# Optimization experiments

Measured on AMD Instinct MI355X. Metric: run time of the kernel, lower is better.

Reference implementation:

```python
import jax, jax.numpy as jnp
import numpy as np

B, T, D, H = 2, 2048, 1024, 16
HD = D // H  # 64
SCALE = 1.0 / np.sqrt(D).astype(np.float32)  # module uses 1/sqrt(mod_dim), not head_dim


def setup_inputs() -> dict:
    key = jax.random.key(0)
    k1, k2, k3 = jax.random.split(key, 3)
    x = jax.random.normal(k1, (B, T, D), dtype=jnp.float32)
    W_attn = jax.random.normal(k2, (3 * D, D), dtype=jnp.float32) * 0.02
    W_out = jax.random.normal(k3, (D, D), dtype=jnp.float32) * 0.02
    return {"x": x, "W_attn": W_attn, "W_out": W_out}


def reference(x, W_attn, W_out):
    b, t, d = x.shape
    # qkv projection (Linear, no bias): x @ W^T
    qkv = jnp.einsum('btd,ed->bte', x, W_attn)  # [b, t, 3d]
    q, k, v = jnp.split(qkv, 3, axis=-1)
    # [b, h, t, hd]
    q = q.reshape(b, t, H, HD).transpose(0, 2, 1, 3)
    k = k.reshape(b, t, H, HD).transpose(0, 2, 1, 3)
    v = v.reshape(b, t, H, HD).transpose(0, 2, 1, 3)
    # raw scores, causal mask applied before scaling (scale*-inf == -inf, so
    # equivalent to the original mask-then-scale order)
    att = jnp.einsum('bhqd,bhkd->bhqk', q, k)
    causal = jnp.tril(jnp.ones((t, t), dtype=bool))
    att = jnp.where(causal[None, None], att * SCALE, -jnp.inf)
    att = jax.nn.softmax(att, axis=-1)
    z = jnp.einsum('bhqk,bhkd->bhqd', att, v)
    z = z.transpose(0, 2, 1, 3).reshape(b, t, d)
    return jnp.einsum('btd,od->bto', z, W_out)
```

## Files before the change

### kernel.cpp

```cpp
#include <hip/hip_runtime.h>
#include <cstddef>

typedef unsigned short u16;
typedef __attribute__((ext_vector_type(4))) float floatx4;
typedef __attribute__((ext_vector_type(8))) short short8;

#define TT 2048
#define DD 1024
#define NH 16
#define ATT_SCALE (1.0f / 32.0f)
#define PSTR 72

__device__ __forceinline__ u16 f2bf(float f) {
  unsigned u = __builtin_bit_cast(unsigned, f);
  u += 0x7fffu + ((u >> 16) & 1u);
  return (u16)(u >> 16);
}

__device__ __forceinline__ void g2l16(const u16* g, u16* l) {
#if __has_builtin(__builtin_amdgcn_global_load_lds)
  __builtin_amdgcn_global_load_lds(
      (const __attribute__((address_space(1))) unsigned int*)g,
      (__attribute__((address_space(3))) unsigned int*)l, 16, 0, 0);
#else
  *(int4*)l = *(const int4*)g;
#endif
}

__device__ __forceinline__ short8 scale_q(short8 q) {
  short8 r;
#pragma unroll
  for (int i = 0; i < 8; ++i) {
    float f = __builtin_bit_cast(float, ((unsigned)(u16)q[i]) << 16) * ATT_SCALE;
    r[i] = (short)f2bf(f);
  }
  return r;
}

__global__ __launch_bounds__(256) void cvt3_kernel(const float* __restrict__ a,
                                                   const float* __restrict__ b,
                                                   const float* __restrict__ c,
                                                   u16* __restrict__ out,
                                                   int na, int nb, int nc) {
  int i = blockIdx.x * 256 + threadIdx.x;
  const float* src;
  int j;
  if (i < na) { src = a; j = i; }
  else if (i < na + nb) { src = b; j = i - na; }
  else if (i < na + nb + nc) { src = c; j = i - na - nb; }
  else return;
  float4 v = ((const float4*)src)[j];
  ((ushort4*)out)[i] = make_ushort4(f2bf(v.x), f2bf(v.y), f2bf(v.z), f2bf(v.w));
}

template <int OUT_BF16, int BN>
__global__ __launch_bounds__(256) void gemm_bt(const u16* __restrict__ A,
                                               const u16* __restrict__ Bm,
                                               void* __restrict__ C,
                                               int M, int N, int K) {
  constexpr int NT = BN / 32;
  __shared__ u16 As[128 * 32];
  __shared__ u16 Bs[BN * 32];
  const int tid = threadIdx.x;
  const int lane = tid & 63;
  const int wave = tid >> 6;
  const int quad = lane >> 4;
  const int l16 = lane & 15;
  const int wm = (wave >> 1) * 64;
  const int wn = (wave & 1) * (BN / 2);
  const int m0 = blockIdx.x * 128;
  const int n0 = blockIdx.y * BN;

  const int srow = wave * 16 + (lane >> 2);
  const int scol = (lane & 3) * 8;
  const int sl = wave * 512 + lane * 8;

  floatx4 acc[4][NT] = {};

  for (int k0 = 0; k0 < K; k0 += 32) {
    __syncthreads();
    g2l16(&A[(size_t)(m0 + srow) * K + k0 + scol], &As[sl]);
    g2l16(&A[(size_t)(m0 + 64 + srow) * K + k0 + scol], &As[2048 + sl]);
    g2l16(&Bm[(size_t)(n0 + srow) * K + k0 + scol], &Bs[sl]);
    if (BN == 128)
      g2l16(&Bm[(size_t)(n0 + 64 + srow) * K + k0 + scol], &Bs[2048 + sl]);
    __syncthreads();

    short8 af[4];
#pragma unroll
    for (int mt = 0; mt < 4; ++mt)
      af[mt] = *(const short8*)&As[(wm + mt * 16 + l16) * 32 + quad * 8];
#pragma unroll
    for (int nt = 0; nt < NT; ++nt) {
      short8 bf = *(const short8*)&Bs[(wn + nt * 16 + l16) * 32 + quad * 8];
#pragma unroll
      for (int mt = 0; mt < 4; ++mt)
        acc[mt][nt] = __builtin_amdgcn_mfma_f32_16x16x32_bf16(af[mt], bf, acc[mt][nt], 0, 0, 0);
    }
  }

#pragma unroll
  for (int mt = 0; mt < 4; ++mt)
#pragma unroll
    for (int nt = 0; nt < NT; ++nt)
#pragma unroll
      for (int r = 0; r < 4; ++r) {
        int gm = m0 + wm + mt * 16 + quad * 4 + r;
        int gn = n0 + wn + nt * 16 + l16;
        float v = acc[mt][nt][r];
        if (OUT_BF16)
          ((u16*)C)[(size_t)gm * N + gn] = f2bf(v);
        else
          ((float*)C)[(size_t)gm * N + gn] = v;
      }
}

__global__ __launch_bounds__(256) void vtrans(const u16* __restrict__ qkv,
                                              u16* __restrict__ vt) {
  __shared__ u16 T[64 * PSTR];
  const int tid = threadIdx.x;
  const int bh = blockIdx.y;
  const int b = bh >> 4, h = bh & 15;
  const int t0 = blockIdx.x * 64;
  const int tr = tid >> 2, c = (tid & 3) * 16;
  const u16* vg = qkv + (size_t)b * TT * 3072 + 2048 + h * 64;
  *(int4*)&T[tr * PSTR + c] = *(const int4*)&vg[(size_t)(t0 + tr) * 3072 + c];
  *(int4*)&T[tr * PSTR + c + 8] = *(const int4*)&vg[(size_t)(t0 + tr) * 3072 + c + 8];
  __syncthreads();
  const int d = tid >> 2, tc = (tid & 3) * 16;
  short8 o0, o1;
#pragma unroll
  for (int j = 0; j < 8; ++j) {
    o0[j] = (short)T[(tc + j) * PSTR + d];
    o1[j] = (short)T[(tc + 8 + j) * PSTR + d];
  }
  u16* dst = vt + ((size_t)bh * 64 + d) * TT + t0 + tc;
  *(short8*)dst = o0;
  *(short8*)(dst + 8) = o1;
}

__global__ __launch_bounds__(256) void attn_flash3(const u16* __restrict__ qkv,
                                                   const u16* __restrict__ vt,
                                                   u16* __restrict__ z) {
  __shared__ u16 Ks[2][64 * PSTR];
  __shared__ u16 Vs[2][64 * PSTR];
  __shared__ u16 Ps[4][2][16 * PSTR];

  const int tid = threadIdx.x;
  const int lane = tid & 63;
  const int wave = tid >> 6;
  const int quad = lane >> 4;
  const int l16 = lane & 15;

  const int p = blockIdx.x;
  const int qtA = p, qtB = 31 - p;
  const int bh = blockIdx.y;
  const int b = bh >> 4, h = bh & 15;

  const size_t bbase = (size_t)b * TT * 3072;
  const u16* qg = qkv + bbase + h * 64;
  const u16* kg = qkv + bbase + 1024 + h * 64;
  const u16* vtg = vt + (size_t)bh * 64 * TT;

  short8 qfA[2], qfB[2];
  {
    const size_t ra = (size_t)(qtA * 64 + wave * 16 + l16) * 3072;
    const size_t rb = (size_t)(qtB * 64 + wave * 16 + l16) * 3072;
    qfA[0] = scale_q(*(const short8*)&qg[ra + quad * 8]);
    qfA[1] = scale_q(*(const short8*)&qg[ra + 32 + quad * 8]);
    qfB[0] = scale_q(*(const short8*)&qg[rb + quad * 8]);
    qfB[1] = scale_q(*(const short8*)&qg[rb + 32 + quad * 8]);
  }

  floatx4 OA[4] = {}, OB[4] = {};
  float psA[4] = {}, psB[4] = {};

  const int str = tid >> 2, sc = (tid & 3) * 16;
  const int nktA = qtA + 1, nktB = qtB + 1;
  const int qrbA = qtA * 64 + wave * 16 + quad * 4;
  const int qrbB = qtB * 64 + wave * 16 + quad * 4;

  {
    int4 k0 = *(const int4*)&kg[(size_t)str * 3072 + sc];
    int4 k1 = *(const int4*)&kg[(size_t)str * 3072 + sc + 8];
    int4 v0 = *(const int4*)&vtg[(size_t)str * TT + sc];
    int4 v1 = *(const int4*)&vtg[(size_t)str * TT + sc + 8];
    *(int4*)&Ks[0][str * PSTR + sc] = k0;
    *(int4*)&Ks[0][str * PSTR + sc + 8] = k1;
    *(int4*)&Vs[0][str * PSTR + sc] = v0;
    *(int4*)&Vs[0][str * PSTR + sc + 8] = v1;
  }
  __syncthreads();

  for (int kt = 0; kt < nktB; ++kt) {
    const int kt0 = kt * 64;
    const int cur = kt & 1, nxt = cur ^ 1;
    const bool pre = (kt + 1 < nktB);

    int4 kr0, kr1, vr0, vr1;
    if (pre) {
      const int kt0n = kt0 + 64;
      kr0 = *(const int4*)&kg[(size_t)(kt0n + str) * 3072 + sc];
      kr1 = *(const int4*)&kg[(size_t)(kt0n + str) * 3072 + sc + 8];
      vr0 = *(const int4*)&vtg[(size_t)str * TT + kt0n + sc];
      vr1 = *(const int4*)&vtg[(size_t)str * TT + kt0n + sc + 8];
    }

    const bool actA = (kt < nktA);

    floatx4 sB[4], sA[4];
#pragma unroll
    for (int nt = 0; nt < 4; ++nt) {
      short8 k0 = *(const short8*)&Ks[cur][(nt * 16 + l16) * PSTR + quad * 8];
      short8 k1 = *(const short8*)&Ks[cur][(nt * 16 + l16) * PSTR + 32 + quad * 8];
      floatx4 zz = {0.f, 0.f, 0.f, 0.f};
      sB[nt] = __builtin_amdgcn_mfma_f32_16x16x32_bf16(qfB[0], k0, zz, 0, 0, 0);
      sB[nt] = __builtin_amdgcn_mfma_f32_16x16x32_bf16(qfB[1], k1, sB[nt], 0, 0, 0);
      if (actA) {
        sA[nt] = __builtin_amdgcn_mfma_f32_16x16x32_bf16(qfA[0], k0, zz, 0, 0, 0);
        sA[nt] = __builtin_amdgcn_mfma_f32_16x16x32_bf16(qfA[1], k1, sA[nt], 0, 0, 0);
      }
    }

    if (kt == qtB) {
#pragma unroll
      for (int nt = 0; nt < 4; ++nt)
#pragma unroll
        for (int r = 0; r < 4; ++r) {
          int kk = kt0 + nt * 16 + l16;
          float pv = (kk <= qrbB + r) ? __expf(sB[nt][r]) : 0.f;
          psB[r] += pv;
          Ps[wave][1][(quad * 4 + r) * PSTR + nt * 16 + l16] = f2bf(pv);
        }
    } else {
#pragma unroll
      for (int nt = 0; nt < 4; ++nt)
#pragma unroll
        for (int r = 0; r < 4; ++r) {
          float pv = __expf(sB[nt][r]);
          psB[r] += pv;
          Ps[wave][1][(quad * 4 + r) * PSTR + nt * 16 + l16] = f2bf(pv);
        }
    }
    if (actA) {
      if (kt == qtA) {
#pragma unroll
        for (int nt = 0; nt < 4; ++nt)
#pragma unroll
          for (int r = 0; r < 4; ++r) {
            int kk = kt0 + nt * 16 + l16;
            float pv = (kk <= qrbA + r) ? __expf(sA[nt][r]) : 0.f;
            psA[r] += pv;
            Ps[wave][0][(quad * 4 + r) * PSTR + nt * 16 + l16] = f2bf(pv);
          }
      } else {
#pragma unroll
        for (int nt = 0; nt < 4; ++nt)
#pragma unroll
          for (int r = 0; r < 4; ++r) {
            float pv = __expf(sA[nt][r]);
            psA[r] += pv;
            Ps[wave][0][(quad * 4 + r) * PSTR + nt * 16 + l16] = f2bf(pv);
          }
      }
    }

    short8 pB0 = *(const short8*)&Ps[wave][1][l16 * PSTR + quad * 8];
    short8 pB1 = *(const short8*)&Ps[wave][1][l16 * PSTR + 32 + quad * 8];
    short8 pA0, pA1;
    if (actA) {
      pA0 = *(const short8*)&Ps[wave][0][l16 * PSTR + quad * 8];
      pA1 = *(const short8*)&Ps[wave][0][l16 * PSTR + 32 + quad * 8];
    }
#pragma unroll
    for (int nt = 0; nt < 4; ++nt) {
      short8 v0 = *(const short8*)&Vs[cur][(nt * 16 + l16) * PSTR + quad * 8];
      short8 v1 = *(const short8*)&Vs[cur][(nt * 16 + l16) * PSTR + 32 + quad * 8];
      OB[nt] = __builtin_amdgcn_mfma_f32_16x16x32_bf16(pB0, v0, OB[nt], 0, 0, 0);
      OB[nt] = __builtin_amdgcn_mfma_f32_16x16x32_bf16(pB1, v1, OB[nt], 0, 0, 0);
      if (actA) {
        OA[nt] = __builtin_amdgcn_mfma_f32_16x16x32_bf16(pA0, v0, OA[nt], 0, 0, 0);
        OA[nt] = __builtin_amdgcn_mfma_f32_16x16x32_bf16(pA1, v1, OA[nt], 0, 0, 0);
      }
    }

    __syncthreads();
    if (pre) {
      *(int4*)&Ks[nxt][str * PSTR + sc] = kr0;
      *(int4*)&Ks[nxt][str * PSTR + sc + 8] = kr1;
      *(int4*)&Vs[nxt][str * PSTR + sc] = vr0;
      *(int4*)&Vs[nxt][str * PSTR + sc + 8] = vr1;
      __syncthreads();
    }
  }

#pragma unroll
  for (int off = 1; off < 16; off <<= 1)
#pragma unroll
    for (int r = 0; r < 4; ++r) {
      psA[r] += __shfl_xor(psA[r], off, 64);
      psB[r] += __shfl_xor(psB[r], off, 64);
    }
#pragma unroll
  for (int r = 0; r < 4; ++r) {
    float rlA = 1.0f / psA[r];
    float rlB = 1.0f / psB[r];
    int qa = qtA * 64 + wave * 16 + quad * 4 + r;
    int qb = qtB * 64 + wave * 16 + quad * 4 + r;
#pragma unroll
    for (int nt = 0; nt < 4; ++nt) {
      int d = nt * 16 + l16;
      z[(size_t)(b * TT + qa) * DD + h * 64 + d] = f2bf(OA[nt][r] * rlA);
      z[(size_t)(b * TT + qb) * DD + h * 64 + d] = f2bf(OB[nt][r] * rlB);
    }
  }
}

extern "C" void kernel_launch(void* const* d_in, const int* in_sizes, int n_in,
                              void* d_out, int out_size, void* d_ws, size_t ws_size,
                              hipStream_t stream) {
  const float* x  = (const float*)d_in[0];
  const float* Wa = (const float*)d_in[1];
  const float* Wo = (const float*)d_in[2];
  float* out = (float*)d_out;

  u16* xb  = (u16*)d_ws;
  u16* Wab = xb  + (size_t)4096 * 1024;
  u16* Wob = Wab + (size_t)3072 * 1024;
  u16* qkv = Wob + (size_t)1024 * 1024;
  u16* z   = qkv + (size_t)4096 * 3072;
  u16* vt  = xb;

  cvt3_kernel<<<8192, 256, 0, stream>>>(x, Wa, Wo, xb,
                                        1048576, 786432, 262144);

  gemm_bt<1, 128><<<dim3(32, 24), 256, 0, stream>>>(xb, Wab, qkv, 4096, 3072, 1024);

  vtrans<<<dim3(TT / 64, 2 * NH), 256, 0, stream>>>(qkv, vt);

  attn_flash3<<<dim3(16, 2 * NH), 256, 0, stream>>>(qkv, vt, z);

  gemm_bt<0, 64><<<dim3(32, 16), 256, 0, stream>>>(z, Wob, out, 4096, 1024, 1024);
}
```

Measured before the change: 188.6 us.

## Fuse V transpose into QKV GEMM epilogue and transpose score MFMA layout

```diff
diff --git a/kernel.cpp b/kernel.cpp
--- a/kernel.cpp
+++ b/kernel.cpp
@@ -15,6 +15,19 @@
   unsigned u = __builtin_bit_cast(unsigned, f);
   u += 0x7fffu + ((u >> 16) & 1u);
   return (u16)(u >> 16);
+}
+
+__device__ __forceinline__ unsigned pack2(float a, float b) {
+#if __has_builtin(__builtin_amdgcn_cvt_pk_bf16_f32)
+  auto t = __builtin_amdgcn_cvt_pk_bf16_f32(a, b);
+  return __builtin_bit_cast(unsigned, t);
+#else
+  unsigned ua = __builtin_bit_cast(unsigned, a);
+  ua += 0x7fffu + ((ua >> 16) & 1u);
+  unsigned ub = __builtin_bit_cast(unsigned, b);
+  ub += 0x7fffu + ((ub >> 16) & 1u);
+  return (ua >> 16) | (ub & 0xffff0000u);
+#endif
 }
 
 __device__ __forceinline__ void g2l16(const u16* g, u16* l) {
@@ -53,10 +66,11 @@
   ((ushort4*)out)[i] = make_ushort4(f2bf(v.x), f2bf(v.y), f2bf(v.z), f2bf(v.w));
 }
 
-template <int OUT_BF16, int BN>
+template <int MODE, int BN>
 __global__ __launch_bounds__(256) void gemm_bt(const u16* __restrict__ A,
                                                const u16* __restrict__ Bm,
                                                void* __restrict__ C,
+                                               u16* __restrict__ vt,
                                                int M, int N, int K) {
   constexpr int NT = BN / 32;
   __shared__ u16 As[128 * 32];
@@ -99,51 +113,45 @@
     }
   }
 
-#pragma unroll
-  for (int mt = 0; mt < 4; ++mt)
-#pragma unroll
-    for (int nt = 0; nt < NT; ++nt)
-#pragma unroll
-      for (int r = 0; r < 4; ++r) {
-        int gm = m0 + wm + mt * 16 + quad * 4 + r;
+  if (MODE == 2 && n0 >= 2048) {
+    const int bidx = m0 >> 11;
+    const int tbase = (m0 & 2047) + wm;
+#pragma unroll
+    for (int mt = 0; mt < 4; ++mt)
+#pragma unroll
+      for (int nt = 0; nt < NT; ++nt) {
         int gn = n0 + wn + nt * 16 + l16;
-        float v = acc[mt][nt][r];
-        if (OUT_BF16)
-          ((u16*)C)[(size_t)gm * N + gn] = f2bf(v);
-        else
-          ((float*)C)[(size_t)gm * N + gn] = v;
-      }
-}
-
-__global__ __launch_bounds__(256) void vtrans(const u16* __restrict__ qkv,
-                                              u16* __restrict__ vt) {
-  __shared__ u16 T[64 * PSTR];
-  const int tid = threadIdx.x;
-  const int bh = blockIdx.y;
-  const int b = bh >> 4, h = bh & 15;
-  const int t0 = blockIdx.x * 64;
-  const int tr = tid >> 2, c = (tid & 3) * 16;
-  const u16* vg = qkv + (size_t)b * TT * 3072 + 2048 + h * 64;
-  *(int4*)&T[tr * PSTR + c] = *(const int4*)&vg[(size_t)(t0 + tr) * 3072 + c];
-  *(int4*)&T[tr * PSTR + c + 8] = *(const int4*)&vg[(size_t)(t0 + tr) * 3072 + c + 8];
-  __syncthreads();
-  const int d = tid >> 2, tc = (tid & 3) * 16;
-  short8 o0, o1;
-#pragma unroll
-  for (int j = 0; j < 8; ++j) {
-    o0[j] = (short)T[(tc + j) * PSTR + d];
-    o1[j] = (short)T[(tc + 8 + j) * PSTR + d];
-  }
-  u16* dst = vt + ((size_t)bh * 64 + d) * TT + t0 + tc;
-  *(short8*)dst = o0;
-  *(short8*)(dst + 8) = o1;
-}
-
-__global__ __launch_bounds__(256) void attn_flash3(const u16* __restrict__ qkv,
+        size_t vrow = (size_t)(bidx * 1024 + gn - 2048);
+        int t = tbase + mt * 16 + quad * 4;
+        uint2 val;
+        val.x = pack2(acc[mt][nt][0], acc[mt][nt][1]);
+        val.y = pack2(acc[mt][nt][2], acc[mt][nt][3]);
+        *(uint2*)&vt[vrow * TT + t] = val;
+      }
+  } else {
+    const int cw = (MODE == 2) ? 2048 : N;
+#pragma unroll
+    for (int mt = 0; mt < 4; ++mt)
+#pragma unroll
+      for (int nt = 0; nt < NT; ++nt)
+#pragma unroll
+        for (int r = 0; r < 4; ++r) {
+          int gm = m0 + wm + mt * 16 + quad * 4 + r;
+          int gn = n0 + wn + nt * 16 + l16;
+          float v = acc[mt][nt][r];
+          if (MODE >= 1)
+            ((u16*)C)[(size_t)gm * cw + gn] = f2bf(v);
+          else
+            ((float*)C)[(size_t)gm * cw + gn] = v;
+        }
+  }
+}
+
+__global__ __launch_bounds__(256) void attn_flash4(const u16* __restrict__ qk,
                                                    const u16* __restrict__ vt,
                                                    u16* __restrict__ z) {
-  __shared__ u16 Ks[2][64 * PSTR];
-  __shared__ u16 Vs[2][64 * PSTR];
+  __shared__ u16 Ks[64 * PSTR];
+  __shared__ u16 Vs[64 * PSTR];
   __shared__ u16 Ps[4][2][16 * PSTR];
 
   const int tid = threadIdx.x;
@@ -157,15 +165,15 @@
   const int bh = blockIdx.y;
   const int b = bh >> 4, h = bh & 15;
 
-  const size_t bbase = (size_t)b * TT * 3072;
-  const u16* qg = qkv + bbase + h * 64;
-  const u16* kg = qkv + bbase + 1024 + h * 64;
+  const size_t bbase = (size_t)b * TT * 2048;
+  const u16* qg = qk + bbase + h * 64;
+  const u16* kg = qk + bbase + 1024 + h * 64;
   const u16* vtg = vt + (size_t)bh * 64 * TT;
 
   short8 qfA[2], qfB[2];
   {
-    const size_t ra = (size_t)(qtA * 64 + wave * 16 + l16) * 3072;
-    const size_t rb = (size_t)(qtB * 64 + wave * 16 + l16) * 3072;
+    const size_t ra = (size_t)(qtA * 64 + wave * 16 + l16) * 2048;
+    const size_t rb = (size_t)(qtB * 64 + wave * 16 + l16) * 2048;
     qfA[0] = scale_q(*(const short8*)&qg[ra + quad * 8]);
     qfA[1] = scale_q(*(const short8*)&qg[ra + 32 + quad * 8]);
     qfB[0] = scale_q(*(const short8*)&qg[rb + quad * 8]);
@@ -173,95 +181,62 @@
   }
 
   floatx4 OA[4] = {}, OB[4] = {};
-  float psA[4] = {}, psB[4] = {};
+  float psA = 0.f, psB = 0.f;
 
   const int str = tid >> 2, sc = (tid & 3) * 16;
   const int nktA = qtA + 1, nktB = qtB + 1;
-  const int qrbA = qtA * 64 + wave * 16 + quad * 4;
-  const int qrbB = qtB * 64 + wave * 16 + quad * 4;
-
-  {
-    int4 k0 = *(const int4*)&kg[(size_t)str * 3072 + sc];
-    int4 k1 = *(const int4*)&kg[(size_t)str * 3072 + sc + 8];
-    int4 v0 = *(const int4*)&vtg[(size_t)str * TT + sc];
-    int4 v1 = *(const int4*)&vtg[(size_t)str * TT + sc + 8];
-    *(int4*)&Ks[0][str * PSTR + sc] = k0;
-    *(int4*)&Ks[0][str * PSTR + sc + 8] = k1;
-    *(int4*)&Vs[0][str * PSTR + sc] = v0;
-    *(int4*)&Vs[0][str * PSTR + sc + 8] = v1;
-  }
-  __syncthreads();
+  const int wl = wave * 16 + l16;
 
   for (int kt = 0; kt < nktB; ++kt) {
     const int kt0 = kt * 64;
-    const int cur = kt & 1, nxt = cur ^ 1;
-    const bool pre = (kt + 1 < nktB);
-
-    int4 kr0, kr1, vr0, vr1;
-    if (pre) {
-      const int kt0n = kt0 + 64;
-      kr0 = *(const int4*)&kg[(size_t)(kt0n + str) * 3072 + sc];
-      kr1 = *(const int4*)&kg[(size_t)(kt0n + str) * 3072 + sc + 8];
-      vr0 = *(const int4*)&vtg[(size_t)str * TT + kt0n + sc];
-      vr1 = *(const int4*)&vtg[(size_t)str * TT + kt0n + sc + 8];
-    }
+    __syncthreads();
+    *(int4*)&Ks[str * PSTR + sc] = *(const int4*)&kg[(size_t)(kt0 + str) * 2048 + sc];
+    *(int4*)&Ks[str * PSTR + sc + 8] = *(const int4*)&kg[(size_t)(kt0 + str) * 2048 + sc + 8];
+    *(int4*)&Vs[str * PSTR + sc] = *(const int4*)&vtg[(size_t)str * TT + kt0 + sc];
+    *(int4*)&Vs[str * PSTR + sc + 8] = *(const int4*)&vtg[(size_t)str * TT + kt0 + sc + 8];
+    __syncthreads();
 
     const bool actA = (kt < nktA);
+    const bool diagA = (kt == qtA), diagB = (kt == qtB);
 
     floatx4 sB[4], sA[4];
 #pragma unroll
     for (int nt = 0; nt < 4; ++nt) {
-      short8 k0 = *(const short8*)&Ks[cur][(nt * 16 + l16) * PSTR + quad * 8];
-      short8 k1 = *(const short8*)&Ks[cur][(nt * 16 + l16) * PSTR + 32 + quad * 8];
+      short8 k0 = *(const short8*)&Ks[(nt * 16 + l16) * PSTR + quad * 8];
+      short8 k1 = *(const short8*)&Ks[(nt * 16 + l16) * PSTR + 32 + quad * 8];
       floatx4 zz = {0.f, 0.f, 0.f, 0.f};
-      sB[nt] = __builtin_amdgcn_mfma_f32_16x16x32_bf16(qfB[0], k0, zz, 0, 0, 0);
-      sB[nt] = __builtin_amdgcn_mfma_f32_16x16x32_bf16(qfB[1], k1, sB[nt], 0, 0, 0);
+      sB[nt] = __builtin_amdgcn_mfma_f32_16x16x32_bf16(k0, qfB[0], zz, 0, 0, 0);
+      sB[nt] = __builtin_amdgcn_mfma_f32_16x16x32_bf16(k1, qfB[1], sB[nt], 0, 0, 0);
       if (actA) {
-        sA[nt] = __builtin_amdgcn_mfma_f32_16x16x32_bf16(qfA[0], k0, zz, 0, 0, 0);
-        sA[nt] = __builtin_amdgcn_mfma_f32_16x16x32_bf16(qfA[1], k1, sA[nt], 0, 0, 0);
-      }
-    }
-
-    if (kt == qtB) {
-#pragma unroll
-      for (int nt = 0; nt < 4; ++nt)
+        sA[nt] = __builtin_amdgcn_mfma_f32_16x16x32_bf16(k0, qfA[0], zz, 0, 0, 0);
+        sA[nt] = __builtin_amdgcn_mfma_f32_16x16x32_bf16(k1, qfA[1], sA[nt], 0, 0, 0);
+      }
+    }
+
+#pragma unroll
+    for (int nt = 0; nt < 4; ++nt) {
+      float e[4];
+#pragma unroll
+      for (int r = 0; r < 4; ++r) {
+        int kl = nt * 16 + quad * 4 + r;
+        e[r] = (!diagB || kl <= wl) ? __expf(sB[nt][r]) : 0.f;
+        psB += e[r];
+      }
+      uint2 val = {pack2(e[0], e[1]), pack2(e[2], e[3])};
+      *(uint2*)&Ps[wave][1][l16 * PSTR + nt * 16 + quad * 4] = val;
+    }
+    if (actA) {
+#pragma unroll
+      for (int nt = 0; nt < 4; ++nt) {
+        float e[4];
 #pragma unroll
         for (int r = 0; r < 4; ++r) {
-          int kk = kt0 + nt * 16 + l16;
-          float pv = (kk <= qrbB + r) ? __expf(sB[nt][r]) : 0.f;
-          psB[r] += pv;
-          Ps[wave][1][(quad * 4 + r) * PSTR + nt * 16 + l16] = f2bf(pv);
+          int kl = nt * 16 + quad * 4 + r;
+          e[r] = (!diagA || kl <= wl) ? __expf(sA[nt][r]) : 0.f;
+          psA += e[r];
         }
-    } else {
-#pragma unroll
-      for (int nt = 0; nt < 4; ++nt)
-#pragma unroll
-        for (int r = 0; r < 4; ++r) {
-          float pv = __expf(sB[nt][r]);
-          psB[r] += pv;
-          Ps[wave][1][(quad * 4 + r) * PSTR + nt * 16 + l16] = f2bf(pv);
-        }
-    }
-    if (actA) {
-      if (kt == qtA) {
-#pragma unroll
-        for (int nt = 0; nt < 4; ++nt)
-#pragma unroll
-          for (int r = 0; r < 4; ++r) {
-            int kk = kt0 + nt * 16 + l16;
-            float pv = (kk <= qrbA + r) ? __expf(sA[nt][r]) : 0.f;
-            psA[r] += pv;
-            Ps[wave][0][(quad * 4 + r) * PSTR + nt * 16 + l16] = f2bf(pv);
-          }
-      } else {
-#pragma unroll
-        for (int nt = 0; nt < 4; ++nt)
-#pragma unroll
-          for (int r = 0; r < 4; ++r) {
-            float pv = __expf(sA[nt][r]);
-            psA[r] += pv;
-            Ps[wave][0][(quad * 4 + r) * PSTR + nt * 16 + l16] = f2bf(pv);
-          }
+        uint2 val = {pack2(e[0], e[1]), pack2(e[2], e[3])};
+        *(uint2*)&Ps[wave][0][l16 * PSTR + nt * 16 + quad * 4] = val;
       }
     }
 
@@ -274,8 +249,8 @@
     }
 #pragma unroll
     for (int nt = 0; nt < 4; ++nt) {
-      short8 v0 = *(const short8*)&Vs[cur][(nt * 16 + l16) * PSTR + quad * 8];
-      short8 v1 = *(const short8*)&Vs[cur][(nt * 16 + l16) * PSTR + 32 + quad * 8];
+      short8 v0 = *(const short8*)&Vs[(nt * 16 + l16) * PSTR + quad * 8];
+      short8 v1 = *(const short8*)&Vs[(nt * 16 + l16) * PSTR + 32 + quad * 8];
       OB[nt] = __builtin_amdgcn_mfma_f32_16x16x32_bf16(pB0, v0, OB[nt], 0, 0, 0);
       OB[nt] = __builtin_amdgcn_mfma_f32_16x16x32_bf16(pB1, v1, OB[nt], 0, 0, 0);
       if (actA) {
@@ -283,28 +258,17 @@
         OA[nt] = __builtin_amdgcn_mfma_f32_16x16x32_bf16(pA1, v1, OA[nt], 0, 0, 0);
       }
     }
-
-    __syncthreads();
-    if (pre) {
-      *(int4*)&Ks[nxt][str * PSTR + sc] = kr0;
-      *(int4*)&Ks[nxt][str * PSTR + sc + 8] = kr1;
-      *(int4*)&Vs[nxt][str * PSTR + sc] = vr0;
-      *(int4*)&Vs[nxt][str * PSTR + sc + 8] = vr1;
-      __syncthreads();
-    }
-  }
-
-#pragma unroll
-  for (int off = 1; off < 16; off <<= 1)
-#pragma unroll
-    for (int r = 0; r < 4; ++r) {
-      psA[r] += __shfl_xor(psA[r], off, 64);
-      psB[r] += __shfl_xor(psB[r], off, 64);
-    }
+  }
+
+  psA += __shfl_xor(psA, 16, 64);
+  psA += __shfl_xor(psA, 32, 64);
+  psB += __shfl_xor(psB, 16, 64);
+  psB += __shfl_xor(psB, 32, 64);
+
 #pragma unroll
   for (int r = 0; r < 4; ++r) {
-    float rlA = 1.0f / psA[r];
-    float rlB = 1.0f / psB[r];
+    float rlA = 1.0f / __shfl(psA, quad * 4 + r, 64);
+    float rlB = 1.0f / __shfl(psB, quad * 4 + r, 64);
     int qa = qtA * 64 + wave * 16 + quad * 4 + r;
     int qb = qtB * 64 + wave * 16 + quad * 4 + r;
 #pragma unroll
@@ -327,18 +291,15 @@
   u16* xb  = (u16*)d_ws;
   u16* Wab = xb  + (size_t)4096 * 1024;
   u16* Wob = Wab + (size_t)3072 * 1024;
-  u16* qkv = Wob + (size_t)1024 * 1024;
-  u16* z   = qkv + (size_t)4096 * 3072;
-  u16* vt  = xb;
-
-  cvt3_kernel<<<8192, 256, 0, stream>>>(x, Wa, Wo, xb,
-                                        1048576, 786432, 262144);
-
-  gemm_bt<1, 128><<<dim3(32, 24), 256, 0, stream>>>(xb, Wab, qkv, 4096, 3072, 1024);
-
-  vtrans<<<dim3(TT / 64, 2 * NH), 256, 0, stream>>>(qkv, vt);
-
-  attn_flash3<<<dim3(16, 2 * NH), 256, 0, stream>>>(qkv, vt, z);
-
-  gemm_bt<0, 64><<<dim3(32, 16), 256, 0, stream>>>(z, Wob, out, 4096, 1024, 1024);
-}
+  u16* qk  = Wob + (size_t)1024 * 1024;
+  u16* z   = qk  + (size_t)4096 * 2048;
+  u16* vt  = z   + (size_t)4096 * 1024;
+
+  cvt3_kernel<<<8192, 256, 0, stream>>>(x, Wa, Wo, xb, 1048576, 786432, 262144);
+
+  gemm_bt<2, 128><<<dim3(32, 24), 256, 0, stream>>>(xb, Wab, qk, vt, 4096, 3072, 1024);
+
+  attn_flash4<<<dim3(16, 2 * NH), 256, 0, stream>>>(qk, vt, z);
+
+  gemm_bt<0, 64><<<dim3(32, 16), 256, 0, stream>>>(z, Wob, out, nullptr, 4096, 1024, 1024);
+}
```

After: 195.5 us. 3.7% more time.
